# Optimization experiments

Hardware: AMD Instinct MI355X
Metric: run time of the kernel (lower is better)

The kernel has to match this reference:

```python
import jax, jax.numpy as jnp
import numpy as np

TEXT_DIM, GIN = 5000, 128
B, N, E = 4096, 200000, 6400000
AE_HID, AE_EMB, G_HID, G_EMB = 8, 4, 8, 4


def _gcn(x, W, b, src, dst):
    N_ = x.shape[0]
    h = x @ W
    loop = jnp.arange(N_)
    s = jnp.concatenate([src, loop])
    d = jnp.concatenate([dst, loop])
    deg = jax.ops.segment_sum(jnp.ones(s.shape[0], h.dtype), d, num_segments=N_)
    dinv = jnp.where(deg > 0, jax.lax.rsqrt(jnp.maximum(deg, 1e-12)), 0.0)
    norm = dinv[s] * dinv[d]
    out = jax.ops.segment_sum(h[s] * norm[:, None], d, num_segments=N_)
    return out + b


def setup_inputs() -> dict:
    key = jax.random.key(0)
    ks = jax.random.split(key, 20)
    def lin(k, fan_in, fan_out):
        lim = 1.0 / np.sqrt(fan_in)
        kw, kb = jax.random.split(k)
        W = jax.random.uniform(kw, (fan_in, fan_out), jnp.float32, -lim, lim)
        b = jax.random.uniform(kb, (fan_out,), jnp.float32, -lim, lim)
        return W, b
    W_e1, b_e1 = lin(ks[0], TEXT_DIM, AE_HID)
    W_e2, b_e2 = lin(ks[1], AE_HID, AE_EMB)
    W_d1, b_d1 = lin(ks[2], AE_EMB, AE_HID)
    W_d2, b_d2 = lin(ks[3], AE_HID, TEXT_DIM)
    W_g1, b_g1 = lin(ks[4], GIN, G_HID)
    W_g2, b_g2 = lin(ks[5], G_HID, G_EMB)
    W_c, b_c = lin(ks[6], AE_EMB + G_EMB, 1)
    text_x = jax.random.normal(ks[7], (B, TEXT_DIM), jnp.float32)
    node_x = jax.random.normal(ks[8], (N, GIN), jnp.float32)
    edge_index = jax.random.randint(ks[9], (2, E), 0, N, jnp.int64 if jax.config.jax_enable_x64 else jnp.int32)
    batch = jnp.sort(jax.random.randint(ks[10], (N,), 0, B, edge_index.dtype))
    return {"text_x": text_x, "node_x": node_x, "edge_index": edge_index, "batch": batch,
            "W_e1": W_e1, "b_e1": b_e1, "W_e2": W_e2, "b_e2": b_e2,
            "W_d1": W_d1, "b_d1": b_d1, "W_d2": W_d2, "b_d2": b_d2,
            "W_g1": W_g1, "b_g1": b_g1, "W_g2": W_g2, "b_g2": b_g2,
            "W_c": W_c, "b_c": b_c}


def reference(text_x, node_x, edge_index, batch,
              W_e1, b_e1, W_e2, b_e2, W_d1, b_d1, W_d2, b_d2,
              W_g1, b_g1, W_g2, b_g2, W_c, b_c):
    # Autoencoder (eval mode: dropout = identity)
    z_text = jax.nn.relu(jax.nn.relu(text_x @ W_e1 + b_e1) @ W_e2 + b_e2)
    x_hat = jax.nn.sigmoid(jax.nn.relu(z_text @ W_d1 + b_d1) @ W_d2 + b_d2)
    # GNN encoder
    src, dst = edge_index[0], edge_index[1]
    h = jax.nn.relu(_gcn(node_x, W_g1, b_g1, src, dst))
    h = _gcn(h, W_g2, b_g2, src, dst)
    # global mean pool over graphs
    nb = text_x.shape[0]
    sums = jax.ops.segment_sum(h, batch, num_segments=nb)
    cnt = jax.ops.segment_sum(jnp.ones(h.shape[0], h.dtype), batch, num_segments=nb)
    z_graph = sums / jnp.maximum(cnt, 1.0)[:, None]
    z = jnp.concatenate([z_text, z_graph], axis=1)
    logits = z @ W_c + b_c
    return (x_hat, logits, z)
```

## Files before the change

### kernel.cpp

```cpp
#include <hip/hip_runtime.h>

#define BB 4096
#define TD 5000
#define NN 200000
#define EE 6400000
#define NBK 782
#define WS_NEED 36881932ull

__global__ void k_init(const int* __restrict__ e, unsigned int* __restrict__ deg,
                       int* __restrict__ flag) {
    int i = blockIdx.x * 256 + threadIdx.x;
    if (i < NN) deg[i] = 1u;
    if (blockIdx.x == 0) {
        __shared__ int r[256];
        int tid = threadIdx.x;
        int acc = 0;
        for (int k = tid; k < 4096; k += 256) acc |= e[2 * k + 1];
        r[tid] = acc;
        __syncthreads();
        for (int s = 128; s > 0; s >>= 1) {
            if (tid < s) r[tid] |= r[tid + s];
            __syncthreads();
        }
        if (tid == 0) *flag = (r[0] == 0) ? 1 : 0;
    }
}

__device__ void role_rank(int rid, int tid, const int* __restrict__ edge,
                          const int* __restrict__ flag, unsigned int* __restrict__ deg,
                          unsigned int* __restrict__ rnkpack) {
    int f = *flag;
    int base = rid * 2048 + tid;
    int d[8];
#pragma unroll
    for (int k = 0; k < 8; k++) {
        int e = base + k * 256;
        d[k] = f ? edge[2 * (EE + e)] : edge[EE + e];
    }
    unsigned int rr[8];
#pragma unroll
    for (int k = 0; k < 8; k++) rr[k] = atomicAdd(&deg[d[k]], 1u);
#pragma unroll
    for (int k = 0; k < 8; k++) rnkpack[base + k * 256] = (rr[k] << 18) | (unsigned int)d[k];
}

__device__ void role_enc(int row, int tid, const float* __restrict__ text,
                         const float* __restrict__ We1, const float* __restrict__ be1,
                         const float* __restrict__ We2, const float* __restrict__ be2,
                         float* __restrict__ z_text) {
    __shared__ float red[8][256];
    __shared__ float t1[8];
    const float4* xrow = (const float4*)(text + (size_t)row * TD);
    float acc[8];
#pragma unroll
    for (int j = 0; j < 8; j++) acc[j] = 0.f;
    for (int v = tid; v < 1250; v += 256) {
        float4 xv = xrow[v];
        const float4* w = (const float4*)(We1 + (size_t)v * 32);
        float xc[4] = {xv.x, xv.y, xv.z, xv.w};
#pragma unroll
        for (int c = 0; c < 4; c++) {
            float4 wa = w[c * 2], wb = w[c * 2 + 1];
            acc[0] += xc[c] * wa.x; acc[1] += xc[c] * wa.y;
            acc[2] += xc[c] * wa.z; acc[3] += xc[c] * wa.w;
            acc[4] += xc[c] * wb.x; acc[5] += xc[c] * wb.y;
            acc[6] += xc[c] * wb.z; acc[7] += xc[c] * wb.w;
        }
    }
#pragma unroll
    for (int j = 0; j < 8; j++) red[j][tid] = acc[j];
    __syncthreads();
    for (int s = 128; s > 0; s >>= 1) {
        if (tid < s) {
#pragma unroll
            for (int j = 0; j < 8; j++) red[j][tid] += red[j][tid + s];
        }
        __syncthreads();
    }
    if (tid < 8) t1[tid] = fmaxf(red[tid][0] + be1[tid], 0.f);
    __syncthreads();
    if (tid < 4) {
        float z = be2[tid];
#pragma unroll
        for (int k = 0; k < 8; k++) z += t1[k] * We2[k * 4 + tid];
        z_text[row * 4 + tid] = fmaxf(z, 0.f);
    }
}

__device__ void role_decode(int row, int tid, const float* __restrict__ zsrc, int zstride,
                            const float* __restrict__ Wd1, const float* __restrict__ bd1,
                            const float* __restrict__ Wd2, const float* __restrict__ bd2,
                            float* __restrict__ xhat) {
    float zz[4];
#pragma unroll
    for (int j = 0; j < 4; j++) zz[j] = zsrc[row * zstride + j];
    float t[8];
#pragma unroll
    for (int k = 0; k < 8; k++) {
        float s = bd1[k];
#pragma unroll
        for (int j = 0; j < 4; j++) s += zz[j] * Wd1[j * 8 + k];
        t[k] = fmaxf(s, 0.f);
    }
    float4* orow = (float4*)(xhat + (size_t)row * TD);
    for (int c4 = tid; c4 < 1250; c4 += 256) {
        float4 s = *(const float4*)(bd2 + c4 * 4);
#pragma unroll
        for (int k = 0; k < 8; k++) {
            float4 w = *(const float4*)(Wd2 + (size_t)k * TD + c4 * 4);
            s.x += t[k] * w.x; s.y += t[k] * w.y;
            s.z += t[k] * w.z; s.w += t[k] * w.w;
        }
        s.x = 1.f / (1.f + expf(-s.x));
        s.y = 1.f / (1.f + expf(-s.y));
        s.z = 1.f / (1.f + expf(-s.z));
        s.w = 1.f / (1.f + expf(-s.w));
        orow[c4] = s;
    }
}

__device__ void role_g1(int gid, int tid, const unsigned int* __restrict__ indptr,
                        const int* __restrict__ csr, const float* __restrict__ h0g,
                        const float* __restrict__ dinv, const float* __restrict__ bg1,
                        const float* __restrict__ Wg2, float* __restrict__ h2g) {
    __shared__ float W[32];
    __shared__ float b1[8];
    __shared__ float h1s[4][8];
    if (tid < 32) W[tid] = Wg2[tid];
    if (tid < 8) b1[tid] = bg1[tid];
    __syncthreads();
    int wid = tid >> 6, lane = tid & 63;
    int i = gid * 4 + wid;
    if (i < NN) {
        int beg = indptr[i], end = indptr[i + 1];
        int f = lane & 7;
        float a = 0.f;
        for (int k = beg + (lane >> 3); k < end; k += 8)
            a += h0g[(size_t)csr[k] * 8 + f];
        a += __shfl_xor(a, 8, 64);
        a += __shfl_xor(a, 16, 64);
        a += __shfl_xor(a, 32, 64);
        if (lane < 8) {
            float di = dinv[i];
            h1s[wid][f] = fmaxf(di * (a + h0g[(size_t)i * 8 + f]) + b1[f], 0.f);
        }
    }
    __syncthreads();
    if (i < NN && lane < 4) {
        float di = dinv[i];
        float s = 0.f;
#pragma unroll
        for (int k = 0; k < 8; k++) s += h1s[wid][k] * W[k * 4 + lane];
        h2g[(size_t)i * 4 + lane] = di * s;
    }
}

__global__ __launch_bounds__(256) void k_fat1(
    const int* __restrict__ edge, const int* __restrict__ flag,
    unsigned int* __restrict__ deg, unsigned int* __restrict__ rnkpack,
    const float* __restrict__ text,
    const float* __restrict__ We1, const float* __restrict__ be1,
    const float* __restrict__ We2, const float* __restrict__ be2,
    float* __restrict__ z_text)
{
    int bid = blockIdx.x, tid = threadIdx.x;
    if (bid < 6250) {
        if (bid & 1) role_enc(bid >> 1, tid, text, We1, be1, We2, be2, z_text);
        else role_rank(bid >> 1, tid, edge, flag, deg, rnkpack);
    } else {
        role_enc(3125 + (bid - 6250), tid, text, We1, be1, We2, be2, z_text);
    }
}

__global__ __launch_bounds__(256) void k_kAmm(
    const unsigned int* __restrict__ deg, const int* __restrict__ batch,
    const int* __restrict__ flag, const float* __restrict__ nodex,
    const float* __restrict__ Wg1, float* __restrict__ dinv,
    unsigned int* __restrict__ bsum, unsigned int* __restrict__ bnd,
    float* __restrict__ h0g)
{
    __shared__ float W[1024];
    __shared__ unsigned int s[256];
    int tid = threadIdx.x;
    for (int i = tid; i < 1024; i += 256) W[i] = Wg1[i];
    int i = blockIdx.x * 256 + tid;
    unsigned int c = 0u;
    float di = 0.f;
    if (i < NN) {
        unsigned int u = deg[i];
        di = rsqrtf((float)u);
        dinv[i] = di;
        c = u - 1u;
        int fg = *flag;
        int b = fg ? batch[2 * i] : batch[i];
        int bp = (i == 0) ? -1 : (fg ? batch[2 * (i - 1)] : batch[i - 1]);
        for (int bb = bp + 1; bb <= b; bb++) bnd[bb] = (unsigned int)i;
        if (i == NN - 1)
            for (int bb = b + 1; bb <= BB; bb++) bnd[bb] = (unsigned int)NN;
    }
    s[tid] = c;
    __syncthreads();
    for (int st = 128; st > 0; st >>= 1) {
        if (tid < st) s[tid] += s[tid + st];
        __syncthreads();
    }
    if (tid == 0) bsum[blockIdx.x] = s[0];
    if (i >= NN) return;
    const float4* xr = (const float4*)(nodex + (size_t)i * 128);
    float acc[8];
#pragma unroll
    for (int j = 0; j < 8; j++) acc[j] = 0.f;
#pragma unroll 8
    for (int c2 = 0; c2 < 32; c2++) {
        float4 v = xr[c2];
        const float* wr = &W[c2 * 32];
#pragma unroll
        for (int j = 0; j < 8; j++)
            acc[j] += v.x * wr[j] + v.y * wr[8 + j] + v.z * wr[16 + j] + v.w * wr[24 + j];
    }
    float* o = h0g + (size_t)i * 8;
#pragma unroll
    for (int j = 0; j < 8; j++) o[j] = di * acc[j];
}

__global__ void kB_scanblocks(const unsigned int* __restrict__ bsum, unsigned int* __restrict__ bpre,
                              unsigned int* __restrict__ indptr) {
    __shared__ unsigned int s[1024];
    int t = threadIdx.x;
    s[t] = (t < NBK) ? bsum[t] : 0u;
    __syncthreads();
    for (int off = 1; off < 1024; off <<= 1) {
        unsigned int v = (t >= off) ? s[t - off] : 0u;
        __syncthreads();
        s[t] += v;
        __syncthreads();
    }
    if (t < NBK) bpre[t] = (t == 0) ? 0u : s[t - 1];
    if (t == 0) indptr[NN] = EE;
}

__global__ void kC_indptr(const unsigned int* __restrict__ deg, const unsigned int* __restrict__ bpre,
                          unsigned int* __restrict__ indptr) {
    __shared__ unsigned int s[256];
    int tid = threadIdx.x;
    int i = blockIdx.x * 256 + tid;
    unsigned int c = (i < NN) ? (deg[i] - 1u) : 0u;
    s[tid] = c;
    __syncthreads();
    for (int off = 1; off < 256; off <<= 1) {
        unsigned int v = (tid >= off) ? s[tid - off] : 0u;
        __syncthreads();
        s[tid] += v;
        __syncthreads();
    }
    if (i < NN) indptr[i] = bpre[blockIdx.x] + s[tid] - c;
}

__global__ __launch_bounds__(256) void k_place(
    const int* __restrict__ edge, const int* __restrict__ flag,
    const unsigned int* __restrict__ indptr, const unsigned int* __restrict__ rnkpack,
    int* __restrict__ csr)
{
    int f = *flag;
    int base = blockIdx.x * 1024 + threadIdx.x;
    int s[4];
    unsigned int p[4];
#pragma unroll
    for (int k = 0; k < 4; k++) {
        int e = base + k * 256;
        s[k] = f ? edge[2 * e] : edge[e];
        p[k] = rnkpack[e];
    }
    unsigned int ip[4];
#pragma unroll
    for (int k = 0; k < 4; k++) ip[k] = indptr[p[k] & 0x3FFFFu];
#pragma unroll
    for (int k = 0; k < 4; k++) csr[ip[k] + (p[k] >> 18) - 1u] = s[k];
}

__global__ __launch_bounds__(256) void k_g1(
    const unsigned int* __restrict__ indptr, const int* __restrict__ csr,
    const float* __restrict__ h0g, const float* __restrict__ dinv,
    const float* __restrict__ bg1, const float* __restrict__ Wg2,
    float* __restrict__ h2g)
{
    role_g1(blockIdx.x, threadIdx.x, indptr, csr, h0g, dinv, bg1, Wg2, h2g);
}

__global__ __launch_bounds__(256) void k_g1_dec(
    const unsigned int* __restrict__ indptr, const int* __restrict__ csr,
    const float* __restrict__ h0g, const float* __restrict__ dinv,
    const float* __restrict__ bg1, const float* __restrict__ Wg2,
    float* __restrict__ h2g,
    const float* __restrict__ z_text,
    const float* __restrict__ Wd1, const float* __restrict__ bd1,
    const float* __restrict__ Wd2, const float* __restrict__ bd2,
    float* __restrict__ xhat)
{
    int bid = blockIdx.x, tid = threadIdx.x;
    if (bid < 8192) {
        if (bid & 1) role_decode(bid >> 1, tid, z_text, 4, Wd1, bd1, Wd2, bd2, xhat);
        else role_g1(bid >> 1, tid, indptr, csr, h0g, dinv, bg1, Wg2, h2g);
    } else {
        role_g1(bid - 4096, tid, indptr, csr, h0g, dinv, bg1, Wg2, h2g);
    }
}

__global__ __launch_bounds__(256) void k_dec(
    const float* __restrict__ zsrc,
    const float* __restrict__ Wd1, const float* __restrict__ bd1,
    const float* __restrict__ Wd2, const float* __restrict__ bd2,
    float* __restrict__ xhat)
{
    role_decode(blockIdx.x, threadIdx.x, zsrc, 8, Wd1, bd1, Wd2, bd2, xhat);
}

__global__ __launch_bounds__(256) void k_gather2(
    const unsigned int* __restrict__ indptr, const int* __restrict__ csr_src,
    const float* __restrict__ h2g, const float* __restrict__ dinv,
    const float* __restrict__ bg2, float* __restrict__ h2f)
{
    __shared__ float b2[4];
    int tid = threadIdx.x;
    if (tid < 4) b2[tid] = bg2[tid];
    __syncthreads();
    int wid = tid >> 6, lane = tid & 63;
    int i = blockIdx.x * 4 + wid;
    if (i >= NN) return;
    int beg = indptr[i], end = indptr[i + 1];
    int f = lane & 3;
    float a = 0.f;
    for (int k = beg + (lane >> 2); k < end; k += 16)
        a += h2g[(size_t)csr_src[k] * 4 + f];
    a += __shfl_xor(a, 4, 64);
    a += __shfl_xor(a, 8, 64);
    a += __shfl_xor(a, 16, 64);
    a += __shfl_xor(a, 32, 64);
    if (lane < 4) {
        float di = dinv[i];
        h2f[(size_t)i * 4 + f] = di * (a + h2g[(size_t)i * 4 + f]) + b2[f];
    }
}

__global__ __launch_bounds__(256) void k_final(
    const float* __restrict__ h2f, const unsigned int* __restrict__ bnd,
    const float* __restrict__ z_text, const float* __restrict__ Wc,
    const float* __restrict__ bc, float* __restrict__ out_logits,
    float* __restrict__ out_z)
{
    __shared__ float red[256][4];
    int g = blockIdx.x, tid = threadIdx.x;
    int lo = bnd[g], hi = bnd[g + 1];
    float a0 = 0.f, a1 = 0.f, a2 = 0.f, a3 = 0.f;
    for (int i = lo + tid; i < hi; i += 256) {
        float4 v = *(const float4*)(h2f + (size_t)i * 4);
        a0 += v.x; a1 += v.y; a2 += v.z; a3 += v.w;
    }
    red[tid][0] = a0; red[tid][1] = a1; red[tid][2] = a2; red[tid][3] = a3;
    __syncthreads();
    for (int s = 128; s > 0; s >>= 1) {
        if (tid < s) {
            red[tid][0] += red[tid + s][0]; red[tid][1] += red[tid + s][1];
            red[tid][2] += red[tid + s][2]; red[tid][3] += red[tid + s][3];
        }
        __syncthreads();
    }
    if (tid == 0) {
        float c = (float)(hi - lo);
        c = fmaxf(c, 1.f);
        float z8[8];
#pragma unroll
        for (int j = 0; j < 4; j++) z8[j] = z_text[g * 4 + j];
#pragma unroll
        for (int j = 0; j < 4; j++) z8[4 + j] = red[0][j] / c;
        float l = bc[0];
#pragma unroll
        for (int k = 0; k < 8; k++) l += z8[k] * Wc[k];
        out_logits[g] = l;
#pragma unroll
        for (int k = 0; k < 8; k++) out_z[g * 8 + k] = z8[k];
    }
}

extern "C" void kernel_launch(void* const* d_in, const int* in_sizes, int n_in,
                              void* d_out, int out_size, void* d_ws, size_t ws_size,
                              hipStream_t stream) {
    const float* text  = (const float*)d_in[0];
    const float* nodex = (const float*)d_in[1];
    const int* edge    = (const int*)d_in[2];
    const int* batch   = (const int*)d_in[3];
    const float* We1 = (const float*)d_in[4];
    const float* be1 = (const float*)d_in[5];
    const float* We2 = (const float*)d_in[6];
    const float* be2 = (const float*)d_in[7];
    const float* Wd1 = (const float*)d_in[8];
    const float* bd1 = (const float*)d_in[9];
    const float* Wd2 = (const float*)d_in[10];
    const float* bd2 = (const float*)d_in[11];
    const float* Wg1 = (const float*)d_in[12];
    const float* bg1 = (const float*)d_in[13];
    const float* Wg2 = (const float*)d_in[14];
    const float* bg2 = (const float*)d_in[15];
    const float* Wc  = (const float*)d_in[16];
    const float* bc  = (const float*)d_in[17];

    float* out_xhat   = (float*)d_out;
    float* out_logits = out_xhat + (size_t)BB * TD;
    float* out_z      = out_logits + BB;

    const bool use_ws = (ws_size >= WS_NEED);

    float *h0g, *h2g, *h2f, *dinv, *z_text;
    unsigned int *deg, *indptr, *rnkpack, *bsum, *bpre, *bnd;
    int *csr, *flag;

    if (use_ws) {
        char* w = (char*)d_ws;
        h0g    = (float*)(w + 0);
        h2f    = h0g;
        h2g    = (float*)(w + 6400000);
        dinv   = (float*)(w + 9600000);
        indptr = (unsigned int*)(w + 10400000);
        csr    = (int*)(w + 11200004);
        z_text = (float*)(w + 36800004);
        bnd    = (unsigned int*)(w + 36865540);
        flag   = (int*)(w + 36881928);
        char* o = (char*)d_out;
        rnkpack = (unsigned int*)(o + 0);
        deg     = (unsigned int*)(o + 25600000);
        bsum    = (unsigned int*)(o + 26400000);
        bpre    = (unsigned int*)(o + 26403128);
    } else {
        char* o = (char*)d_out;
        h0g     = (float*)(o + 0);
        h2g     = (float*)(o + 6400000);
        h2f     = (float*)(o + 9600000);
        dinv    = (float*)(o + 12800000);
        deg     = (unsigned int*)(o + 13600000);
        indptr  = (unsigned int*)(o + 14400000);
        rnkpack = (unsigned int*)(o + 15200004);
        csr     = (int*)(o + 40800004);
        bsum    = (unsigned int*)(o + 66400004);
        bpre    = (unsigned int*)(o + 66403132);
        z_text  = (float*)(o + 66406260);
        bnd     = (unsigned int*)(o + 66471796);
        flag    = (int*)(o + 66488184);
    }

    k_init<<<NBK, 256, 0, stream>>>(edge, deg, flag);
    k_fat1<<<7221, 256, 0, stream>>>(edge, flag, deg, rnkpack,
                                     text, We1, be1, We2, be2, z_text);
    k_kAmm<<<NBK, 256, 0, stream>>>(deg, batch, flag, nodex, Wg1,
                                    dinv, bsum, bnd, h0g);
    kB_scanblocks<<<1, 1024, 0, stream>>>(bsum, bpre, indptr);
    kC_indptr<<<NBK, 256, 0, stream>>>(deg, bpre, indptr);
    k_place<<<6250, 256, 0, stream>>>(edge, flag, indptr, rnkpack, csr);

    if (use_ws) {
        k_g1_dec<<<54096, 256, 0, stream>>>(indptr, csr, h0g, dinv, bg1, Wg2, h2g,
                                            z_text, Wd1, bd1, Wd2, bd2, out_xhat);
    } else {
        k_g1<<<(NN + 3) / 4, 256, 0, stream>>>(indptr, csr, h0g, dinv, bg1, Wg2, h2g);
    }

    k_gather2<<<(NN + 3) / 4, 256, 0, stream>>>(indptr, csr, h2g, dinv, bg2, h2f);
    k_final<<<BB, 256, 0, stream>>>(h2f, bnd, z_text, Wc, bc, out_logits, out_z);

    if (!use_ws) {
        k_dec<<<BB, 256, 0, stream>>>(out_z, Wd1, bd1, Wd2, bd2, out_xhat);
    }
}
```

Before: 746.0 us.

## Restructure pipeline: inline dtype detection, single-block scan, fuse decode with CSR placement

Drops the init kernel by zeroing degrees with a memset and detecting int64 edge indices per wavefront with shuffles. The two-kernel block scan for indptr is replaced by one extra block in the node kernel that serially scans degrees in 256 chunks. The decoder now runs alongside CSR placement instead of the first GCN layer, and the workspace layout moves rnkpack and csr into the workspace, which needs a larger workspace. Kernel launches are fewer, but the single-block serial scan of 200k entries may sit on the critical path.

```diff
diff --git a/kernel.cpp b/kernel.cpp
--- a/kernel.cpp
+++ b/kernel.cpp
@@ -5,31 +5,18 @@
 #define NN 200000
 #define EE 6400000
 #define NBK 782
-#define WS_NEED 36881932ull
-
-__global__ void k_init(const int* __restrict__ e, unsigned int* __restrict__ deg,
-                       int* __restrict__ flag) {
-    int i = blockIdx.x * 256 + threadIdx.x;
-    if (i < NN) deg[i] = 1u;
-    if (blockIdx.x == 0) {
-        __shared__ int r[256];
-        int tid = threadIdx.x;
-        int acc = 0;
-        for (int k = tid; k < 4096; k += 256) acc |= e[2 * k + 1];
-        r[tid] = acc;
-        __syncthreads();
-        for (int s = 128; s > 0; s >>= 1) {
-            if (tid < s) r[tid] |= r[tid + s];
-            __syncthreads();
-        }
-        if (tid == 0) *flag = (r[0] == 0) ? 1 : 0;
-    }
+#define WS_NEED 62481928ull
+
+__device__ __forceinline__ int detect_i64(const int* __restrict__ e) {
+    int v = e[2 * (threadIdx.x & 63) + 1];
+#pragma unroll
+    for (int off = 32; off >= 1; off >>= 1) v |= __shfl_xor(v, off, 64);
+    return v == 0;
 }
 
 __device__ void role_rank(int rid, int tid, const int* __restrict__ edge,
-                          const int* __restrict__ flag, unsigned int* __restrict__ deg,
-                          unsigned int* __restrict__ rnkpack) {
-    int f = *flag;
+                          unsigned int* __restrict__ deg, unsigned int* __restrict__ rnkpack) {
+    int f = detect_i64(edge);
     int base = rid * 2048 + tid;
     int d[8];
 #pragma unroll
@@ -117,6 +104,26 @@
         s.w = 1.f / (1.f + expf(-s.w));
         orow[c4] = s;
     }
+}
+
+__device__ void role_place(int pid, int tid, const int* __restrict__ edge,
+                           const unsigned int* __restrict__ indptr,
+                           const unsigned int* __restrict__ rnkpack, int* __restrict__ csr) {
+    int f = detect_i64(edge);
+    int base = pid * 1024 + tid;
+    int s[4];
+    unsigned int p[4];
+#pragma unroll
+    for (int k = 0; k < 4; k++) {
+        int e = base + k * 256;
+        s[k] = f ? edge[2 * e] : edge[e];
+        p[k] = rnkpack[e];
+    }
+    unsigned int ip[4];
+#pragma unroll
+    for (int k = 0; k < 4; k++) ip[k] = indptr[p[k] & 0x3FFFFu];
+#pragma unroll
+    for (int k = 0; k < 4; k++) csr[ip[k] + (p[k] >> 18)] = s[k];
 }
 
 __device__ void role_g1(int gid, int tid, const unsigned int* __restrict__ indptr,
@@ -156,9 +163,8 @@
 }
 
 __global__ __launch_bounds__(256) void k_fat1(
-    const int* __restrict__ edge, const int* __restrict__ flag,
-    unsigned int* __restrict__ deg, unsigned int* __restrict__ rnkpack,
-    const float* __restrict__ text,
+    const int* __restrict__ edge, unsigned int* __restrict__ deg,
+    unsigned int* __restrict__ rnkpack, const float* __restrict__ text,
     const float* __restrict__ We1, const float* __restrict__ be1,
     const float* __restrict__ We2, const float* __restrict__ be2,
     float* __restrict__ z_text)
@@ -166,45 +172,55 @@
     int bid = blockIdx.x, tid = threadIdx.x;
     if (bid < 6250) {
         if (bid & 1) role_enc(bid >> 1, tid, text, We1, be1, We2, be2, z_text);
-        else role_rank(bid >> 1, tid, edge, flag, deg, rnkpack);
+        else role_rank(bid >> 1, tid, edge, deg, rnkpack);
     } else {
         role_enc(3125 + (bid - 6250), tid, text, We1, be1, We2, be2, z_text);
     }
 }
 
-__global__ __launch_bounds__(256) void k_kAmm(
+__global__ __launch_bounds__(256) void k_node(
     const unsigned int* __restrict__ deg, const int* __restrict__ batch,
-    const int* __restrict__ flag, const float* __restrict__ nodex,
+    const int* __restrict__ edge, const float* __restrict__ nodex,
     const float* __restrict__ Wg1, float* __restrict__ dinv,
-    unsigned int* __restrict__ bsum, unsigned int* __restrict__ bnd,
-    float* __restrict__ h0g)
-{
+    unsigned int* __restrict__ bnd, float* __restrict__ h0g,
+    unsigned int* __restrict__ indptr)
+{
+    int bid = blockIdx.x, tid = threadIdx.x;
+    if (bid == NBK) {
+        __shared__ unsigned int ps[256];
+        const int CH = 782;
+        int lo = tid * CH, hi = min(lo + CH, NN);
+        unsigned int s = 0;
+        for (int i = lo; i < hi; i++) s += deg[i];
+        ps[tid] = s;
+        __syncthreads();
+        for (int off = 1; off < 256; off <<= 1) {
+            unsigned int v = (tid >= off) ? ps[tid - off] : 0u;
+            __syncthreads();
+            ps[tid] += v;
+            __syncthreads();
+        }
+        unsigned int run = (tid == 0) ? 0u : ps[tid - 1];
+        for (int i = lo; i < hi; i++) { indptr[i] = run; run += deg[i]; }
+        if (tid == 255) indptr[NN] = run;
+        return;
+    }
     __shared__ float W[1024];
-    __shared__ unsigned int s[256];
-    int tid = threadIdx.x;
     for (int i = tid; i < 1024; i += 256) W[i] = Wg1[i];
-    int i = blockIdx.x * 256 + tid;
-    unsigned int c = 0u;
+    int i = bid * 256 + tid;
+    int f = detect_i64(edge);
     float di = 0.f;
     if (i < NN) {
         unsigned int u = deg[i];
-        di = rsqrtf((float)u);
+        di = rsqrtf((float)(u + 1u));
         dinv[i] = di;
-        c = u - 1u;
-        int fg = *flag;
-        int b = fg ? batch[2 * i] : batch[i];
-        int bp = (i == 0) ? -1 : (fg ? batch[2 * (i - 1)] : batch[i - 1]);
+        int b = f ? batch[2 * i] : batch[i];
+        int bp = (i == 0) ? -1 : (f ? batch[2 * (i - 1)] : batch[i - 1]);
         for (int bb = bp + 1; bb <= b; bb++) bnd[bb] = (unsigned int)i;
         if (i == NN - 1)
             for (int bb = b + 1; bb <= BB; bb++) bnd[bb] = (unsigned int)NN;
     }
-    s[tid] = c;
-    __syncthreads();
-    for (int st = 128; st > 0; st >>= 1) {
-        if (tid < st) s[tid] += s[tid + st];
-        __syncthreads();
-    }
-    if (tid == 0) bsum[blockIdx.x] = s[0];
+    __syncthreads();
     if (i >= NN) return;
     const float4* xr = (const float4*)(nodex + (size_t)i * 128);
     float acc[8];
@@ -223,59 +239,28 @@
     for (int j = 0; j < 8; j++) o[j] = di * acc[j];
 }
 
-__global__ void kB_scanblocks(const unsigned int* __restrict__ bsum, unsigned int* __restrict__ bpre,
-                              unsigned int* __restrict__ indptr) {
-    __shared__ unsigned int s[1024];
-    int t = threadIdx.x;
-    s[t] = (t < NBK) ? bsum[t] : 0u;
-    __syncthreads();
-    for (int off = 1; off < 1024; off <<= 1) {
-        unsigned int v = (t >= off) ? s[t - off] : 0u;
-        __syncthreads();
-        s[t] += v;
-        __syncthreads();
-    }
-    if (t < NBK) bpre[t] = (t == 0) ? 0u : s[t - 1];
-    if (t == 0) indptr[NN] = EE;
-}
-
-__global__ void kC_indptr(const unsigned int* __restrict__ deg, const unsigned int* __restrict__ bpre,
-                          unsigned int* __restrict__ indptr) {
-    __shared__ unsigned int s[256];
-    int tid = threadIdx.x;
-    int i = blockIdx.x * 256 + tid;
-    unsigned int c = (i < NN) ? (deg[i] - 1u) : 0u;
-    s[tid] = c;
-    __syncthreads();
-    for (int off = 1; off < 256; off <<= 1) {
-        unsigned int v = (tid >= off) ? s[tid - off] : 0u;
-        __syncthreads();
-        s[tid] += v;
-        __syncthreads();
-    }
-    if (i < NN) indptr[i] = bpre[blockIdx.x] + s[tid] - c;
-}
-
 __global__ __launch_bounds__(256) void k_place(
-    const int* __restrict__ edge, const int* __restrict__ flag,
-    const unsigned int* __restrict__ indptr, const unsigned int* __restrict__ rnkpack,
-    int* __restrict__ csr)
-{
-    int f = *flag;
-    int base = blockIdx.x * 1024 + threadIdx.x;
-    int s[4];
-    unsigned int p[4];
-#pragma unroll
-    for (int k = 0; k < 4; k++) {
-        int e = base + k * 256;
-        s[k] = f ? edge[2 * e] : edge[e];
-        p[k] = rnkpack[e];
-    }
-    unsigned int ip[4];
-#pragma unroll
-    for (int k = 0; k < 4; k++) ip[k] = indptr[p[k] & 0x3FFFFu];
-#pragma unroll
-    for (int k = 0; k < 4; k++) csr[ip[k] + (p[k] >> 18) - 1u] = s[k];
+    const int* __restrict__ edge, const unsigned int* __restrict__ indptr,
+    const unsigned int* __restrict__ rnkpack, int* __restrict__ csr)
+{
+    role_place(blockIdx.x, threadIdx.x, edge, indptr, rnkpack, csr);
+}
+
+__global__ __launch_bounds__(256) void k_place_dec(
+    const int* __restrict__ edge, const unsigned int* __restrict__ indptr,
+    const unsigned int* __restrict__ rnkpack, int* __restrict__ csr,
+    const float* __restrict__ z_text,
+    const float* __restrict__ Wd1, const float* __restrict__ bd1,
+    const float* __restrict__ Wd2, const float* __restrict__ bd2,
+    float* __restrict__ xhat)
+{
+    int bid = blockIdx.x, tid = threadIdx.x;
+    if (bid < 8192) {
+        if (bid & 1) role_decode(bid >> 1, tid, z_text, 4, Wd1, bd1, Wd2, bd2, xhat);
+        else role_place(bid >> 1, tid, edge, indptr, rnkpack, csr);
+    } else {
+        role_place(4096 + (bid - 8192), tid, edge, indptr, rnkpack, csr);
+    }
 }
 
 __global__ __launch_bounds__(256) void k_g1(
@@ -285,25 +270,6 @@
     float* __restrict__ h2g)
 {
     role_g1(blockIdx.x, threadIdx.x, indptr, csr, h0g, dinv, bg1, Wg2, h2g);
-}
-
-__global__ __launch_bounds__(256) void k_g1_dec(
-    const unsigned int* __restrict__ indptr, const int* __restrict__ csr,
-    const float* __restrict__ h0g, const float* __restrict__ dinv,
-    const float* __restrict__ bg1, const float* __restrict__ Wg2,
-    float* __restrict__ h2g,
-    const float* __restrict__ z_text,
-    const float* __restrict__ Wd1, const float* __restrict__ bd1,
-    const float* __restrict__ Wd2, const float* __restrict__ bd2,
-    float* __restrict__ xhat)
-{
-    int bid = blockIdx.x, tid = threadIdx.x;
-    if (bid < 8192) {
-        if (bid & 1) role_decode(bid >> 1, tid, z_text, 4, Wd1, bd1, Wd2, bd2, xhat);
-        else role_g1(bid >> 1, tid, indptr, csr, h0g, dinv, bg1, Wg2, h2g);
-    } else {
-        role_g1(bid - 4096, tid, indptr, csr, h0g, dinv, bg1, Wg2, h2g);
-    }
 }
 
 __global__ __launch_bounds__(256) void k_dec(
@@ -411,25 +377,21 @@
     const bool use_ws = (ws_size >= WS_NEED);
 
     float *h0g, *h2g, *h2f, *dinv, *z_text;
-    unsigned int *deg, *indptr, *rnkpack, *bsum, *bpre, *bnd;
-    int *csr, *flag;
+    unsigned int *deg, *indptr, *rnkpack, *bnd;
+    int *csr;
 
     if (use_ws) {
         char* w = (char*)d_ws;
-        h0g    = (float*)(w + 0);
-        h2f    = h0g;
-        h2g    = (float*)(w + 6400000);
-        dinv   = (float*)(w + 9600000);
-        indptr = (unsigned int*)(w + 10400000);
-        csr    = (int*)(w + 11200004);
-        z_text = (float*)(w + 36800004);
-        bnd    = (unsigned int*)(w + 36865540);
-        flag   = (int*)(w + 36881928);
-        char* o = (char*)d_out;
-        rnkpack = (unsigned int*)(o + 0);
-        deg     = (unsigned int*)(o + 25600000);
-        bsum    = (unsigned int*)(o + 26400000);
-        bpre    = (unsigned int*)(o + 26403128);
+        rnkpack = (unsigned int*)(w + 0);
+        csr     = (int*)(w + 25600000);
+        h0g     = (float*)(w + 51200000);
+        h2f     = h0g;
+        h2g     = (float*)(w + 57600000);
+        dinv    = (float*)(w + 60800000);
+        indptr  = (unsigned int*)(w + 61600000);
+        z_text  = (float*)(w + 62400004);
+        bnd     = (unsigned int*)(w + 62465540);
+        deg     = (unsigned int*)d_out;
     } else {
         char* o = (char*)d_out;
         h0g     = (float*)(o + 0);
@@ -440,29 +402,25 @@
         indptr  = (unsigned int*)(o + 14400000);
         rnkpack = (unsigned int*)(o + 15200004);
         csr     = (int*)(o + 40800004);
-        bsum    = (unsigned int*)(o + 66400004);
-        bpre    = (unsigned int*)(o + 66403132);
-        z_text  = (float*)(o + 66406260);
-        bnd     = (unsigned int*)(o + 66471796);
-        flag    = (int*)(o + 66488184);
-    }
-
-    k_init<<<NBK, 256, 0, stream>>>(edge, deg, flag);
-    k_fat1<<<7221, 256, 0, stream>>>(edge, flag, deg, rnkpack,
-                                     text, We1, be1, We2, be2, z_text);
-    k_kAmm<<<NBK, 256, 0, stream>>>(deg, batch, flag, nodex, Wg1,
-                                    dinv, bsum, bnd, h0g);
-    kB_scanblocks<<<1, 1024, 0, stream>>>(bsum, bpre, indptr);
-    kC_indptr<<<NBK, 256, 0, stream>>>(deg, bpre, indptr);
-    k_place<<<6250, 256, 0, stream>>>(edge, flag, indptr, rnkpack, csr);
+        z_text  = (float*)(o + 66400008);
+        bnd     = (unsigned int*)(o + 66465544);
+    }
+
+    hipMemsetAsync(deg, 0, NN * sizeof(unsigned int), stream);
+
+    k_fat1<<<7221, 256, use_ws ? 1024 : 0, stream>>>(edge, deg, rnkpack,
+                                                     text, We1, be1, We2, be2, z_text);
+    k_node<<<NBK + 1, 256, 0, stream>>>(deg, batch, edge, nodex, Wg1,
+                                        dinv, bnd, h0g, indptr);
 
     if (use_ws) {
-        k_g1_dec<<<54096, 256, 0, stream>>>(indptr, csr, h0g, dinv, bg1, Wg2, h2g,
-                                            z_text, Wd1, bd1, Wd2, bd2, out_xhat);
+        k_place_dec<<<10346, 256, 0, stream>>>(edge, indptr, rnkpack, csr,
+                                               z_text, Wd1, bd1, Wd2, bd2, out_xhat);
     } else {
-        k_g1<<<(NN + 3) / 4, 256, 0, stream>>>(indptr, csr, h0g, dinv, bg1, Wg2, h2g);
-    }
-
+        k_place<<<6250, 256, 0, stream>>>(edge, indptr, rnkpack, csr);
+    }
+
+    k_g1<<<(NN + 3) / 4, 256, 0, stream>>>(indptr, csr, h0g, dinv, bg1, Wg2, h2g);
     k_gather2<<<(NN + 3) / 4, 256, 0, stream>>>(indptr, csr, h2g, dinv, bg2, h2f);
     k_final<<<BB, 256, 0, stream>>>(h2f, bnd, z_text, Wc, bc, out_logits, out_z);
 
```

After: 1.067 ms. +43.0%, slower.
